# Performance work log

Measured on AMD Instinct MI355X. Metric: run time of the kernel, lower is better.

## Reference

```python
import jax, jax.numpy as jnp
import numpy as np

N = 100000   # nodes
E = 1600000  # edges (avg degree 16)
D = 64       # embedding_dim
H = 64       # hidden_dim


def setup_inputs() -> dict:
    key = jax.random.key(0)
    k = jax.random.split(key, 4)
    embedding = jax.random.normal(k[0], (N, D), dtype=jnp.float32)
    edge_index = jax.random.randint(k[1], (2, E), 0, N, dtype=jnp.int64)
    W1 = jax.random.normal(k[2], (D, H), dtype=jnp.float32) / np.sqrt(D).astype(np.float32)
    b1 = jnp.zeros((H,), jnp.float32)
    W2 = jax.random.normal(k[3], (H, D), dtype=jnp.float32) / np.sqrt(H).astype(np.float32)
    b2 = jnp.zeros((D,), jnp.float32)
    return {"embedding": embedding, "edge_index": edge_index,
            "W1": W1, "b1": b1, "W2": W2, "b2": b2}


def _gcn_layer(x, src, dst, norm, W, b, n):
    # linear transform first (small GEMM), then normalized scatter-add aggregation
    h = x @ W                                   # [n, out]
    msg = h[src] * norm[:, None]                # gather + scale, [E+n, out]
    out = jax.ops.segment_sum(msg, dst, num_segments=n)
    return out + b


def reference(embedding, edge_index, W1, b1, W2, b2):
    n = embedding.shape[0]
    loop = jnp.arange(n)
    # GCNConv adds self-loops before normalization
    src = jnp.concatenate([edge_index[0], loop])
    dst = jnp.concatenate([edge_index[1], loop])
    deg = jax.ops.segment_sum(jnp.ones_like(dst, dtype=embedding.dtype), dst, num_segments=n)
    dinv = jax.lax.rsqrt(deg)                   # deg >= 1 thanks to self-loops
    norm = dinv[src] * dinv[dst]                # symmetric D^-1/2 A_hat D^-1/2
    h1 = jax.nn.relu(_gcn_layer(embedding, src, dst, norm, W1, b1, n))
    h2 = jax.nn.relu(_gcn_layer(h1, src, dst, norm, W2, b2, n))
    return h2
```

## Files before the change

### kernel.cpp

```cpp
#include <hip/hip_runtime.h>
#include <hip/hip_fp16.h>


#define NBMAX 512
#define BCAP  5120
#define CHUNK 8192

__global__ void zero_int_kernel(int* __restrict__ p, int m) {
    int i = blockIdx.x * blockDim.x + threadIdx.x;
    if (i < m) p[i] = 0;
}

__global__ __launch_bounds__(512) void bucket_scatter_kernel(
        const int* __restrict__ src, const int* __restrict__ dst,
        int* __restrict__ bucket_fill, unsigned int* __restrict__ bucketed,
        int E, int nb) {
    __shared__ int cnt[NBMAX];
    __shared__ int sc[NBMAX];
    __shared__ int exc[NBMAX + 1];
    __shared__ int rk[NBMAX];
    __shared__ int gb[NBMAX];
    __shared__ unsigned int pk[CHUNK];
    __shared__ unsigned short bid[CHUNK];
    int t = threadIdx.x;
    int base = blockIdx.x * CHUNK;
    cnt[t] = 0; rk[t] = 0;
    __syncthreads();
    unsigned int s[16]; int b[16];
#pragma unroll
    for (int j = 0; j < 16; ++j) {
        int e = base + j * 512 + t;
        if (e < E) {
            int d = dst[e];
            b[j] = d >> 8;
            s[j] = (unsigned int)src[e] | ((unsigned int)(d & 255) << 17);
            atomicAdd(&cnt[b[j]], 1);
        } else b[j] = -1;
    }
    __syncthreads();
    sc[t] = cnt[t];
    __syncthreads();
    for (int off = 1; off < NBMAX; off <<= 1) {
        int x = (t >= off) ? sc[t - off] : 0;
        __syncthreads();
        sc[t] += x;
        __syncthreads();
    }
    if (t == 0) exc[0] = 0;
    exc[t + 1] = sc[t];
    __syncthreads();
#pragma unroll
    for (int j = 0; j < 16; ++j) {
        if (b[j] >= 0) {
            int r = atomicAdd(&rk[b[j]], 1);
            int pos = exc[b[j]] + r;
            pk[pos] = s[j];
            bid[pos] = (unsigned short)b[j];
        }
    }
    if (t < nb && cnt[t] > 0) gb[t] = atomicAdd(&bucket_fill[t], cnt[t]);
    __syncthreads();
    int m = exc[NBMAX];
    for (int idx = t; idx < m; idx += 512) {
        int bb = bid[idx];
        int off = gb[bb] + (idx - exc[bb]);
        if (off < BCAP) bucketed[(size_t)bb * BCAP + off] = pk[idx];
    }
}

__global__ void bucket_scan_kernel(const int* __restrict__ bucket_fill,
                                   int* __restrict__ bucket_base,
                                   int* __restrict__ row_ptr, int nb, int n) {
    __shared__ int sm[NBMAX];
    int t = threadIdx.x;
    int v = (t < nb) ? bucket_fill[t] : 0;
    sm[t] = v; __syncthreads();
    for (int off = 1; off < NBMAX; off <<= 1) {
        int x = (t >= off) ? sm[t - off] : 0;
        __syncthreads();
        sm[t] += x;
        __syncthreads();
    }
    if (t < nb) bucket_base[t] = sm[t] - v;
    if (t == nb - 1) { bucket_base[nb] = sm[t]; row_ptr[n] = sm[t]; }
}

__global__ __launch_bounds__(256) void csr_build_kernel(
        const unsigned int* __restrict__ bucketed, const int* __restrict__ bucket_fill,
        const int* __restrict__ bucket_base, int* __restrict__ row_ptr,
        float* __restrict__ dinv, int* __restrict__ col_src, int n) {
    __shared__ int cnt[256], rk2[256], sc2[256], lofs[256];
    __shared__ unsigned int ent[BCAP];
    __shared__ int cout[BCAP];
    int b = blockIdx.x, t = threadIdx.x;
    int m = bucket_fill[b]; if (m > BCAP) m = BCAP;
    int gbase = bucket_base[b];
    cnt[t] = 0; rk2[t] = 0;
    __syncthreads();
    const unsigned int* ebase = bucketed + (size_t)b * BCAP;
    for (int i = t; i < m; i += 256) {
        unsigned int p = ebase[i];
        ent[i] = p;
        atomicAdd(&cnt[p >> 17], 1);
    }
    __syncthreads();
    int v = cnt[t];
    sc2[t] = v; __syncthreads();
    for (int off = 1; off < 256; off <<= 1) {
        int x = (t >= off) ? sc2[t - off] : 0;
        __syncthreads();
        sc2[t] += x;
        __syncthreads();
    }
    lofs[t] = sc2[t] - v;
    __syncthreads();
    int node = (b << 8) + t;
    if (node < n) {
        row_ptr[node] = gbase + lofs[t];
        dinv[node] = rsqrtf((float)(v + 1));
    }
    for (int i = t; i < m; i += 256) {
        unsigned int p = ent[i];
        int dl = p >> 17;
        int r = atomicAdd(&rk2[dl], 1);
        cout[lofs[dl] + r] = (int)(p & 0x1FFFF);
    }
    __syncthreads();
    for (int i = t; i < m; i += 256) col_src[gbase + i] = cout[i];
}

__global__ __launch_bounds__(256, 4) void gemm_scale_kernel(
        const float* __restrict__ x, const float* __restrict__ W,
        const float* __restrict__ dinv, __half* __restrict__ g, int n) {
    __shared__ float4 ws4[64 * 16];
    int t = threadIdx.x;
    const float4* W4 = (const float4*)W;
#pragma unroll
    for (int j = 0; j < 4; ++j) ws4[j * 256 + t] = W4[j * 256 + t];
    __syncthreads();
    int cg = t & 7;
    int rg = t >> 3;
    int row0 = blockIdx.x * 128;
    const float4* x4 = (const float4*)x;
    int r[4];
#pragma unroll
    for (int j = 0; j < 4; ++j) {
        int rr = row0 + rg + 32 * j;
        r[j] = (rr < n) ? rr : 0;
    }
    float4 acc[4][2];
#pragma unroll
    for (int j = 0; j < 4; ++j) {
        acc[j][0] = make_float4(0.f, 0.f, 0.f, 0.f);
        acc[j][1] = make_float4(0.f, 0.f, 0.f, 0.f);
    }
#pragma unroll 2
    for (int kq = 0; kq < 16; ++kq) {
        float4 xv[4];
#pragma unroll
        for (int j = 0; j < 4; ++j) xv[j] = x4[(size_t)r[j] * 16 + kq];
#pragma unroll
        for (int kk = 0; kk < 4; ++kk) {
            int k = kq * 4 + kk;
            float4 w0 = ws4[k * 16 + 2 * cg];
            float4 w1 = ws4[k * 16 + 2 * cg + 1];
#pragma unroll
            for (int j = 0; j < 4; ++j) {
                float xk = ((const float*)&xv[j])[kk];
                acc[j][0].x = fmaf(xk, w0.x, acc[j][0].x);
                acc[j][0].y = fmaf(xk, w0.y, acc[j][0].y);
                acc[j][0].z = fmaf(xk, w0.z, acc[j][0].z);
                acc[j][0].w = fmaf(xk, w0.w, acc[j][0].w);
                acc[j][1].x = fmaf(xk, w1.x, acc[j][1].x);
                acc[j][1].y = fmaf(xk, w1.y, acc[j][1].y);
                acc[j][1].z = fmaf(xk, w1.z, acc[j][1].z);
                acc[j][1].w = fmaf(xk, w1.w, acc[j][1].w);
            }
        }
    }
    uint4* g16 = (uint4*)g;
#pragma unroll
    for (int j = 0; j < 4; ++j) {
        int rr = row0 + rg + 32 * j;
        if (rr < n) {
            float d = dinv[rr];
            __half2 h0 = __floats2half2_rn(acc[j][0].x * d, acc[j][0].y * d);
            __half2 h1 = __floats2half2_rn(acc[j][0].z * d, acc[j][0].w * d);
            __half2 h2 = __floats2half2_rn(acc[j][1].x * d, acc[j][1].y * d);
            __half2 h3 = __floats2half2_rn(acc[j][1].z * d, acc[j][1].w * d);
            uint4 u;
            u.x = *(unsigned int*)&h0;
            u.y = *(unsigned int*)&h1;
            u.z = *(unsigned int*)&h2;
            u.w = *(unsigned int*)&h3;
            g16[(size_t)rr * 8 + cg] = u;
        }
    }
}

__device__ __forceinline__ void acc_add_h8(float* acc, uint4 u) {
    const __half2* hp = (const __half2*)&u;
#pragma unroll
    for (int q = 0; q < 4; ++q) {
        float2 f = __half22float2(hp[q]);
        acc[2 * q]     += f.x;
        acc[2 * q + 1] += f.y;
    }
}

__global__ __launch_bounds__(256) void aggregate_kernel(
        const __half* __restrict__ g, const int* __restrict__ row_ptr,
        const int* __restrict__ col_src, const float* __restrict__ dinv,
        const float* __restrict__ bias, float* __restrict__ out, int n) {
    int wid = (blockIdx.x * 256 + threadIdx.x) >> 6;
    int lane = threadIdx.x & 63;
    int grp = lane >> 3;
    int l8  = lane & 7;
    if (wid >= n) return;
    const uint4* g16 = (const uint4*)g;
    float acc[8] = {0.f, 0.f, 0.f, 0.f, 0.f, 0.f, 0.f, 0.f};
    int beg = row_ptr[wid];
    int end = row_ptr[wid + 1];
    int i = beg + grp;
    for (; i + 8 < end; i += 16) {
        int s0 = col_src[i];
        int s1 = col_src[i + 8];
        uint4 u0 = g16[(size_t)s0 * 8 + l8];
        uint4 u1 = g16[(size_t)s1 * 8 + l8];
        acc_add_h8(acc, u0);
        acc_add_h8(acc, u1);
    }
    for (; i < end; i += 8) {
        int s = col_src[i];
        uint4 u = g16[(size_t)s * 8 + l8];
        acc_add_h8(acc, u);
    }
#pragma unroll
    for (int c = 0; c < 8; ++c) {
        acc[c] += __shfl_xor(acc[c], 8, 64);
        acc[c] += __shfl_xor(acc[c], 16, 64);
        acc[c] += __shfl_xor(acc[c], 32, 64);
    }
    if (grp == 0) {
        uint4 us = g16[(size_t)wid * 8 + l8];
        acc_add_h8(acc, us);
        float d = dinv[wid];
        const float4* b4 = (const float4*)bias;
        float4 ba = b4[2 * l8], bb = b4[2 * l8 + 1];
        float4 o0, o1;
        o0.x = fmaxf(fmaf(acc[0], d, ba.x), 0.f);
        o0.y = fmaxf(fmaf(acc[1], d, ba.y), 0.f);
        o0.z = fmaxf(fmaf(acc[2], d, ba.z), 0.f);
        o0.w = fmaxf(fmaf(acc[3], d, ba.w), 0.f);
        o1.x = fmaxf(fmaf(acc[4], d, bb.x), 0.f);
        o1.y = fmaxf(fmaf(acc[5], d, bb.y), 0.f);
        o1.z = fmaxf(fmaf(acc[6], d, bb.z), 0.f);
        o1.w = fmaxf(fmaf(acc[7], d, bb.w), 0.f);
        float4* o4 = (float4*)out;
        o4[(size_t)wid * 16 + 2 * l8]     = o0;
        o4[(size_t)wid * 16 + 2 * l8 + 1] = o1;
    }
}

extern "C" void kernel_launch(void* const* d_in, const int* in_sizes, int n_in,
                              void* d_out, int out_size, void* d_ws, size_t ws_size,
                              hipStream_t stream) {
    const float* embedding = (const float*)d_in[0];
    const int*   edge_idx  = (const int*)d_in[1];
    const float* W1        = (const float*)d_in[2];
    const float* b1        = (const float*)d_in[3];
    const float* W2        = (const float*)d_in[4];
    const float* b2        = (const float*)d_in[5];
    float* out = (float*)d_out;

    const int n = in_sizes[0] / 64;
    const int E = in_sizes[1] / 2;
    const int* src = edge_idx;
    const int* dst = edge_idx + E;
    const int nb = (n + 255) >> 8;

    char* w = (char*)d_ws;
    auto alloc = [&](size_t bytes) {
        char* p = w;
        w += (bytes + 255) & ~(size_t)255;
        return p;
    };
    int*   row_ptr     = (int*)  alloc(((size_t)n + 1) * 4);
    float* dinv        = (float*)alloc((size_t)n * 4);
    int*   col_src     = (int*)  alloc((size_t)E * 4);
    int*   bucket_fill = (int*)  alloc((size_t)nb * 4);
    int*   bucket_base = (int*)  alloc(((size_t)nb + 1) * 4);
    char*  gshare      = alloc((size_t)n * 64 * 4);
    __half* g          = (__half*)gshare;
    unsigned int* bucketed = (unsigned int*)gshare;

    zero_int_kernel<<<(nb + 255) / 256, 256, 0, stream>>>(bucket_fill, nb);
    bucket_scatter_kernel<<<(E + CHUNK - 1) / CHUNK, 512, 0, stream>>>(
        src, dst, bucket_fill, bucketed, E, nb);
    bucket_scan_kernel<<<1, NBMAX, 0, stream>>>(bucket_fill, bucket_base, row_ptr, nb, n);
    csr_build_kernel<<<nb, 256, 0, stream>>>(
        bucketed, bucket_fill, bucket_base, row_ptr, dinv, col_src, n);

    const int gemm_blocks = (n + 127) / 128;
    const int agg_blocks  = (int)(((size_t)n * 64 + 255) / 256);

    gemm_scale_kernel<<<gemm_blocks, 256, 0, stream>>>(embedding, W1, dinv, g, n);
    aggregate_kernel<<<agg_blocks, 256, 0, stream>>>(g, row_ptr, col_src, dinv, b1, out, n);
    gemm_scale_kernel<<<gemm_blocks, 256, 0, stream>>>(out, W2, dinv, g, n);
    aggregate_kernel<<<agg_blocks, 256, 0, stream>>>(g, row_ptr, col_src, dinv, b2, out, n);
}
```

Before: 240.6 us.

## Fold bucket scan into CSR build, memset zeroing, half2 pre-add in aggregation

Removes the separate zero kernel (replaced by hipMemsetAsync) and the single-block bucket scan kernel, so each CSR-build block now recomputes the 512-entry prefix scan redundantly in shared memory. CSR build no longer stages bucket entries in LDS and instead re-reads them from global memory in the second pass. The aggregation inner loop adds pairs of gathered fp16 rows in half2 before converting to fp32, halving the conversions but accumulating partly in half precision. These aim to cut launch count and LDS usage at the cost of redundant scan work, extra global reads and some precision loss.

```diff
diff --git a/kernel.cpp b/kernel.cpp
--- a/kernel.cpp
+++ b/kernel.cpp
@@ -5,11 +5,6 @@
 #define NBMAX 512
 #define BCAP  5120
 #define CHUNK 8192
-
-__global__ void zero_int_kernel(int* __restrict__ p, int m) {
-    int i = blockIdx.x * blockDim.x + threadIdx.x;
-    if (i < m) p[i] = 0;
-}
 
 __global__ __launch_bounds__(512) void bucket_scatter_kernel(
         const int* __restrict__ src, const int* __restrict__ dst,
@@ -68,41 +63,36 @@
     }
 }
 
-__global__ void bucket_scan_kernel(const int* __restrict__ bucket_fill,
-                                   int* __restrict__ bucket_base,
-                                   int* __restrict__ row_ptr, int nb, int n) {
-    __shared__ int sm[NBMAX];
-    int t = threadIdx.x;
-    int v = (t < nb) ? bucket_fill[t] : 0;
-    sm[t] = v; __syncthreads();
-    for (int off = 1; off < NBMAX; off <<= 1) {
-        int x = (t >= off) ? sm[t - off] : 0;
-        __syncthreads();
-        sm[t] += x;
-        __syncthreads();
-    }
-    if (t < nb) bucket_base[t] = sm[t] - v;
-    if (t == nb - 1) { bucket_base[nb] = sm[t]; row_ptr[n] = sm[t]; }
-}
-
 __global__ __launch_bounds__(256) void csr_build_kernel(
         const unsigned int* __restrict__ bucketed, const int* __restrict__ bucket_fill,
-        const int* __restrict__ bucket_base, int* __restrict__ row_ptr,
-        float* __restrict__ dinv, int* __restrict__ col_src, int n) {
+        int* __restrict__ row_ptr, float* __restrict__ dinv,
+        int* __restrict__ col_src, int n, int nb) {
+    __shared__ int bf[NBMAX];
+    __shared__ int sc[NBMAX];
     __shared__ int cnt[256], rk2[256], sc2[256], lofs[256];
-    __shared__ unsigned int ent[BCAP];
     __shared__ int cout[BCAP];
     int b = blockIdx.x, t = threadIdx.x;
-    int m = bucket_fill[b]; if (m > BCAP) m = BCAP;
-    int gbase = bucket_base[b];
+    bf[t]       = (t < nb)       ? bucket_fill[t]       : 0;
+    bf[t + 256] = (t + 256 < nb) ? bucket_fill[t + 256] : 0;
+    __syncthreads();
+    sc[t] = bf[t];
+    sc[t + 256] = bf[t + 256];
+    __syncthreads();
+    for (int off = 1; off < NBMAX; off <<= 1) {
+        int v0 = (t >= off) ? sc[t - off] : 0;
+        int v1 = sc[t + 256 - off];
+        __syncthreads();
+        sc[t] += v0; sc[t + 256] += v1;
+        __syncthreads();
+    }
     cnt[t] = 0; rk2[t] = 0;
     __syncthreads();
+    if (b == 0 && t == 0) row_ptr[n] = sc[nb - 1];
+    int m = bf[b]; if (m > BCAP) m = BCAP;
+    int gbase = sc[b] - bf[b];
     const unsigned int* ebase = bucketed + (size_t)b * BCAP;
-    for (int i = t; i < m; i += 256) {
-        unsigned int p = ebase[i];
-        ent[i] = p;
-        atomicAdd(&cnt[p >> 17], 1);
-    }
+    for (int i = t; i < m; i += 256)
+        atomicAdd(&cnt[ebase[i] >> 17], 1);
     __syncthreads();
     int v = cnt[t];
     sc2[t] = v; __syncthreads();
@@ -120,7 +110,7 @@
         dinv[node] = rsqrtf((float)(v + 1));
     }
     for (int i = t; i < m; i += 256) {
-        unsigned int p = ent[i];
+        unsigned int p = ebase[i];
         int dl = p >> 17;
         int r = atomicAdd(&rk2[dl], 1);
         cout[lofs[dl] + r] = (int)(p & 0x1FFFF);
@@ -227,8 +217,15 @@
         int s1 = col_src[i + 8];
         uint4 u0 = g16[(size_t)s0 * 8 + l8];
         uint4 u1 = g16[(size_t)s1 * 8 + l8];
-        acc_add_h8(acc, u0);
-        acc_add_h8(acc, u1);
+        const __half2* a = (const __half2*)&u0;
+        const __half2* b = (const __half2*)&u1;
+#pragma unroll
+        for (int q = 0; q < 4; ++q) {
+            __half2 sph = __hadd2(a[q], b[q]);
+            float2 f = __half22float2(sph);
+            acc[2 * q]     += f.x;
+            acc[2 * q + 1] += f.y;
+        }
     }
     for (; i < end; i += 8) {
         int s = col_src[i];
@@ -289,17 +286,15 @@
     float* dinv        = (float*)alloc((size_t)n * 4);
     int*   col_src     = (int*)  alloc((size_t)E * 4);
     int*   bucket_fill = (int*)  alloc((size_t)nb * 4);
-    int*   bucket_base = (int*)  alloc(((size_t)nb + 1) * 4);
     char*  gshare      = alloc((size_t)n * 64 * 4);
     __half* g          = (__half*)gshare;
     unsigned int* bucketed = (unsigned int*)gshare;
 
-    zero_int_kernel<<<(nb + 255) / 256, 256, 0, stream>>>(bucket_fill, nb);
+    hipMemsetAsync(bucket_fill, 0, (size_t)nb * 4, stream);
     bucket_scatter_kernel<<<(E + CHUNK - 1) / CHUNK, 512, 0, stream>>>(
         src, dst, bucket_fill, bucketed, E, nb);
-    bucket_scan_kernel<<<1, NBMAX, 0, stream>>>(bucket_fill, bucket_base, row_ptr, nb, n);
     csr_build_kernel<<<nb, 256, 0, stream>>>(
-        bucketed, bucket_fill, bucket_base, row_ptr, dinv, col_src, n);
+        bucketed, bucket_fill, row_ptr, dinv, col_src, n, nb);
 
     const int gemm_blocks = (n + 127) / 128;
     const int agg_blocks  = (int)(((size_t)n * 64 + 255) / 256);
```

Measured after the change: 241.2 us. Within noise of the previous version (+0.2%).
